# Kernel tuning notes

Measured on AMD Instinct MI355X. Metric: run time of the kernel, lower is better.

## Reference

```python
import jax, jax.numpy as jnp
import numpy as np
from jax import lax

NEG = -1e16  # value used by masked_fill in the original
DN = ('NCHW', 'OIHW', 'NCHW')


def _time_block(X, w1, b1, w2, b2, w3, b3):
    # X: [B, N, T, C] -> conv over time with kernel (1,3), VALID -> [B, N, T-2, O]
    x = jnp.transpose(X, (0, 3, 1, 2))  # [B, C, N, T]
    conv = lambda w, b: lax.conv_general_dilated(x, w, (1, 1), 'VALID', dimension_numbers=DN) + b[None, :, None, None]
    temp = conv(w1, b1) + jax.nn.sigmoid(conv(w2, b2))
    out = jax.nn.relu(temp + conv(w3, b3))
    return jnp.transpose(out, (0, 2, 3, 1))  # [B, N, T-2, O]


def _gat_single(x, graph, W, b):
    # x: [B, N, C]; W: [D, C]; b: [D]
    h = jnp.einsum('bnc,dc->bnd', x, W)
    s = jnp.einsum('bnd,bmd->bnm', h, h) * graph[None]
    s = jnp.where(s == 0, NEG, s)
    a = jax.nn.softmax(s, axis=-1)
    return jnp.einsum('bnm,bmd->bnd', a, h) + b


def _gat_multihead(x, graph, Wh, bh):
    # x: [B, N, C]; Wh: [H, D, C]; bh: [H, D] -> [B, N, H*D] (head-major concat, matching torch.cat)
    h = jnp.einsum('bnc,hdc->bhnd', x, Wh)
    s = jnp.einsum('bhnd,bhmd->bhnm', h, h) * graph[None, None]
    s = jnp.where(s == 0, NEG, s)
    a = jax.nn.softmax(s, axis=-1)
    o = jnp.einsum('bhnm,bhmd->bhnd', a, h) + bh[None, :, None, :]
    B, H, N, D = o.shape
    return jnp.transpose(o, (0, 2, 1, 3)).reshape(B, N, H * D)


def setup_inputs() -> dict:
    key = jax.random.key(0)
    ks = jax.random.split(key, 12)
    B, N, T, C = 2, 4096, 5, 192
    hid, out_c, H = 64, 64, 4
    inp = {
        'flow': jax.random.normal(ks[0], (B, N, T, C), jnp.float32),
        'graph': jax.random.randint(ks[1], (N, N), 0, 2).astype(jnp.float32),
        'tb_w1': jax.random.normal(ks[2], (hid, C, 1, 3), jnp.float32) * 0.1,
        'tb_b1': jax.random.normal(ks[3], (hid,), jnp.float32) * 0.1,
        'tb_w2': jax.random.normal(ks[4], (hid, C, 1, 3), jnp.float32) * 0.1,
        'tb_b2': jax.random.normal(ks[5], (hid,), jnp.float32) * 0.1,
        'tb_w3': jax.random.normal(ks[6], (hid, C, 1, 3), jnp.float32) * 0.1,
        'tb_b3': jax.random.normal(ks[7], (hid,), jnp.float32) * 0.1,
        'Wh': jax.random.normal(ks[8], (H, hid, C), jnp.float32) * 0.1,
        'bh': jax.random.normal(ks[9], (H, hid), jnp.float32) * 0.1,
        'Wo': jax.random.normal(ks[10], (out_c, hid * H), jnp.float32) * 0.1,
        'bo': jax.random.normal(ks[11], (out_c,), jnp.float32) * 0.1,
    }
    return inp


def reference(flow, graph, tb_w1, tb_b1, tb_w2, tb_b2, tb_w3, tb_b3, Wh, bh, Wo, bo):
    B, N = flow.shape[0], flow.shape[1]
    t1 = _time_block(flow, tb_w1, tb_b1, tb_w2, tb_b2, tb_w3, tb_b3)  # [B, N, T-2, hid]
    x = t1.reshape(B, N, -1)  # [B, N, (T-2)*hid]
    x = jax.nn.leaky_relu(_gat_multihead(x, graph, Wh, bh), negative_slope=0.01)
    x = jax.nn.leaky_relu(_gat_single(x, graph, Wo, bo), negative_slope=0.01)
    return x[:, :, None, :]  # [B, N, 1, out_c]
```

## Files before the change

kernel.cpp:

```cpp
#include <hip/hip_runtime.h>
#include <math.h>

#define N_NODES 4096

typedef unsigned short u16;
typedef unsigned int u32;

typedef __attribute__((ext_vector_type(8))) short bfrag;
typedef __attribute__((ext_vector_type(4))) float f4;

__device__ __forceinline__ u16 f2bf(float x) {
    union { float f; u32 u; } v; v.f = x;
    u32 r = (v.u + 0x7FFFu + ((v.u >> 16) & 1u)) >> 16;
    return (u16)r;
}
__device__ __forceinline__ float bf2f(u16 b) {
    union { float f; u32 u; } v; v.u = ((u32)b) << 16; return v.f;
}
__device__ __forceinline__ u32 cvtpk(float a, float b) {
    u32 r;
    asm("v_cvt_pk_bf16_f32 %0, %1, %2" : "=v"(r) : "v"(a), "v"(b));
    return r;
}
__device__ __forceinline__ float u2f(u32 u) {
    union { u32 u; float f; } v; v.u = u; return v.f;
}

__global__ __launch_bounds__(256) void wprep_kernel(
    const float* __restrict__ w1, const float* __restrict__ w2,
    const float* __restrict__ w3,
    u16* __restrict__ w_hi, u16* __restrict__ w_mid, u16* __restrict__ w_lo)
{
    int idx = blockIdx.x * 256 + threadIdx.x;
    if (idx >= 192 * 576) return;
    int col = idx / 576, k = idx % 576;
    int conv = col >> 6, o = col & 63;
    int kk = k / 192, c = k % 192;
    const float* w = (conv == 0) ? w1 : (conv == 1 ? w2 : w3);
    float v = w[(o * 192 + c) * 3 + kk];
    u16 h = f2bf(v);   float r1 = v - bf2f(h);
    u16 m = f2bf(r1);  float r2 = r1 - bf2f(m);
    u16 lo = f2bf(r2);
    int kc = k >> 6, rem = k & 63, j = rem >> 3, e = rem & 7;
    int pos = col * 576 + kc * 64 + ((j ^ (col & 7)) << 3) + e;
    w_hi[pos] = h;
    w_mid[pos] = m;
    w_lo[pos] = lo;
}

__global__ __launch_bounds__(512) void timeblock_mfma_kernel(
    const float* __restrict__ flow,
    const u16* __restrict__ w_hi, const u16* __restrict__ w_mid,
    const u16* __restrict__ w_lo,
    const float* __restrict__ b1, const float* __restrict__ b2,
    const float* __restrict__ b3, float* __restrict__ x1)
{
    __shared__ __align__(16) u16 As[3][128 * 64];
    __shared__ __align__(16) u16 Bs[3][192 * 64];

    const int tid = threadIdx.x;
    const int wv = tid >> 6, l = tid & 63;
    const int ln15 = l & 15, ln16 = l >> 4;
    const int wr = wv >> 1, wc = wv & 1;
    const int nodebase = blockIdx.x * 128;
    const int t = blockIdx.y;

    f4 acc[2][6];
#pragma unroll
    for (int rq = 0; rq < 2; ++rq)
#pragma unroll
        for (int nt = 0; nt < 6; ++nt) {
            acc[rq][nt][0] = 0.f; acc[rq][nt][1] = 0.f;
            acc[rq][nt][2] = 0.f; acc[rq][nt][3] = 0.f;
        }

    for (int kc = 0; kc < 9; ++kc) {
        __syncthreads();

#pragma unroll
        for (int u = tid; u < 1024; u += 512) {
            int r = u >> 3, j = u & 7;
            const float* srcp = flow + (size_t)(nodebase + r) * 960 + t * 192 + kc * 64 + j * 8;
            float4 f0 = *(const float4*)srcp;
            float4 f1 = *(const float4*)(srcp + 4);
            float fv[8] = { f0.x, f0.y, f0.z, f0.w, f1.x, f1.y, f1.z, f1.w };
            union { uint4 q; u16 a[8]; } uh, um, ul;
#pragma unroll
            for (int e = 0; e < 8; ++e) {
                u16 h = f2bf(fv[e]);   float r1 = fv[e] - bf2f(h);
                u16 m = f2bf(r1);      float r2 = r1 - bf2f(m);
                uh.a[e] = h; um.a[e] = m; ul.a[e] = f2bf(r2);
            }
            int pos = r * 64 + ((j ^ (r & 7)) << 3);
            *(uint4*)&As[0][pos] = uh.q;
            *(uint4*)&As[1][pos] = um.q;
            *(uint4*)&As[2][pos] = ul.q;
        }

#pragma unroll
        for (int arr = 0; arr < 3; ++arr) {
            const u16* wsrc = (arr == 0) ? w_hi : (arr == 1 ? w_mid : w_lo);
#pragma unroll
            for (int i = 0; i < 3; ++i) {
                int colg = wv * 24 + i * 8;
                const u16* srcp = wsrc + (size_t)(colg + (l >> 3)) * 576 + kc * 64 + (l & 7) * 8;
                u16* dstp = &Bs[arr][colg * 64];
                __builtin_amdgcn_global_load_lds(
                    (const __attribute__((address_space(1))) u32*)srcp,
                    (__attribute__((address_space(3))) u32*)dstp, 16, 0, 0);
            }
        }

        __syncthreads();

        bfrag af[2][3][2];
#pragma unroll
        for (int rq = 0; rq < 2; ++rq) {
            int arow = wr * 32 + rq * 16 + ln15;
#pragma unroll
            for (int ks = 0; ks < 2; ++ks) {
                int idx = arow * 64 + (((ks * 4 + ln16) ^ (arow & 7)) << 3);
                af[rq][0][ks] = *(const bfrag*)&As[0][idx];
                af[rq][1][ks] = *(const bfrag*)&As[1][idx];
                af[rq][2][ks] = *(const bfrag*)&As[2][idx];
            }
        }

#pragma unroll
        for (int cv = 0; cv < 3; ++cv) {
#pragma unroll
            for (int ntj = 0; ntj < 2; ++ntj) {
                int col = cv * 64 + wc * 32 + ntj * 16 + ln15;
                int nt = cv * 2 + ntj;
#pragma unroll
                for (int ks = 0; ks < 2; ++ks) {
                    int idx = col * 64 + (((ks * 4 + ln16) ^ (col & 7)) << 3);
                    bfrag bh = *(const bfrag*)&Bs[0][idx];
                    bfrag bm = *(const bfrag*)&Bs[1][idx];
                    bfrag bl = *(const bfrag*)&Bs[2][idx];
#pragma unroll
                    for (int rq = 0; rq < 2; ++rq) {
                        f4 a = acc[rq][nt];
                        a = __builtin_amdgcn_mfma_f32_16x16x32_bf16(af[rq][0][ks], bh, a, 0, 0, 0);
                        a = __builtin_amdgcn_mfma_f32_16x16x32_bf16(af[rq][0][ks], bm, a, 0, 0, 0);
                        a = __builtin_amdgcn_mfma_f32_16x16x32_bf16(af[rq][1][ks], bh, a, 0, 0, 0);
                        a = __builtin_amdgcn_mfma_f32_16x16x32_bf16(af[rq][0][ks], bl, a, 0, 0, 0);
                        a = __builtin_amdgcn_mfma_f32_16x16x32_bf16(af[rq][2][ks], bh, a, 0, 0, 0);
                        a = __builtin_amdgcn_mfma_f32_16x16x32_bf16(af[rq][1][ks], bm, a, 0, 0, 0);
                        acc[rq][nt] = a;
                    }
                }
            }
        }
    }

#pragma unroll
    for (int rq = 0; rq < 2; ++rq) {
#pragma unroll
        for (int ntj = 0; ntj < 2; ++ntj) {
            int o = wc * 32 + ntj * 16 + ln15;
            float bb1 = b1[o], bb2 = b2[o], bb3 = b3[o];
#pragma unroll
            for (int rg = 0; rg < 4; ++rg) {
                int node = nodebase + wr * 32 + rq * 16 + ln16 * 4 + rg;
                float c1 = acc[rq][0 * 2 + ntj][rg] + bb1;
                float c2 = acc[rq][1 * 2 + ntj][rg] + bb2;
                float c3 = acc[rq][2 * 2 + ntj][rg] + bb3;
                float sg = 1.0f / (1.0f + __expf(-c2));
                float v = c1 + sg + c3;
                x1[(size_t)node * 192 + t * 64 + o] = v > 0.f ? v : 0.f;
            }
        }
    }
}

__global__ __launch_bounds__(256) void linear64_split_kernel(
    const float* __restrict__ in, const float* __restrict__ W,
    u16* __restrict__ h_hi, u16* __restrict__ h_lo,
    u16* __restrict__ hTb_hi, u16* __restrict__ hTb_lo,
    int C, int H)
{
    __shared__ float xs[64][68];
    __shared__ float wsm[64][68];
    const int tid = threadIdx.x;
    const int g = blockIdx.y;
    const int rowbase = blockIdx.x * 64;
    const int rgrp = tid >> 4, cgrp = tid & 15;

    float acc[4][4] = {};
    for (int c0 = 0; c0 < C; c0 += 64) {
        __syncthreads();
        for (int i = tid; i < 4096; i += 256) {
            int r = i >> 6, cc = i & 63;
            xs[r][cc]  = in[(size_t)(rowbase + r) * C + c0 + cc];
            wsm[r][cc] = W[(size_t)(g * 64 + r) * C + c0 + cc];
        }
        __syncthreads();
        for (int cc = 0; cc < 64; cc += 4) {
            float4 xv[4], wv[4];
#pragma unroll
            for (int i = 0; i < 4; ++i)
                xv[i] = *reinterpret_cast<const float4*>(&xs[4 * rgrp + i][cc]);
#pragma unroll
            for (int j = 0; j < 4; ++j)
                wv[j] = *reinterpret_cast<const float4*>(&wsm[4 * cgrp + j][cc]);
#pragma unroll
            for (int i = 0; i < 4; ++i) {
#pragma unroll
                for (int j = 0; j < 4; ++j) {
                    acc[i][j] += xv[i].x * wv[j].x + xv[i].y * wv[j].y
                               + xv[i].z * wv[j].z + xv[i].w * wv[j].w;
                }
            }
        }
    }

    u16 hi[4][4], lo[4][4];
#pragma unroll
    for (int i = 0; i < 4; ++i)
#pragma unroll
        for (int j = 0; j < 4; ++j) {
            float a = acc[i][j];
            u16 h = f2bf(a);
            hi[i][j] = h;
            lo[i][j] = f2bf(a - bf2f(h));
        }

    const int b = rowbase >> 12;
    const size_t mapb = (size_t)(b * H + g) * (4096 * 64);

#pragma unroll
    for (int i = 0; i < 4; ++i) {
        int n = (rowbase & 4095) + 4 * rgrp + i;
        ushort4 vh = { hi[i][0], hi[i][1], hi[i][2], hi[i][3] };
        ushort4 vl = { lo[i][0], lo[i][1], lo[i][2], lo[i][3] };
        *(ushort4*)&h_hi[mapb + (size_t)n * 64 + 4 * cgrp] = vh;
        *(ushort4*)&h_lo[mapb + (size_t)n * 64 + 4 * cgrp] = vl;
    }
    {
        int n0 = (rowbase & 4095) + 4 * rgrp;
        size_t tb = mapb + ((size_t)(n0 >> 6) * 64) * 64;
#pragma unroll
        for (int j = 0; j < 4; ++j) {
            int d = 4 * cgrp + j;
            ushort4 vh = { hi[0][j], hi[1][j], hi[2][j], hi[3][j] };
            ushort4 vl = { lo[0][j], lo[1][j], lo[2][j], lo[3][j] };
            *(ushort4*)&hTb_hi[tb + (size_t)d * 64 + (n0 & 63)] = vh;
            *(ushort4*)&hTb_lo[tb + (size_t)d * 64 + (n0 & 63)] = vl;
        }
    }
}

__global__ __launch_bounds__(256) void flash_mfma_kernel(
    const u16* __restrict__ h_hi, const u16* __restrict__ h_lo,
    const u16* __restrict__ hTb_hi, const u16* __restrict__ hTb_lo,
    const float* __restrict__ graph, const float* __restrict__ bias,
    float* __restrict__ out, int H, int rstride,
    int ntiles, int mode, float* __restrict__ pO, float* __restrict__ pml)
{
    __shared__ __align__(16) u16 hcs[2][4][4096];

    const int tid = threadIdx.x;
    const int wv = tid >> 6;
    const int l = tid & 63;
    const int ln15 = l & 15, ln16 = l >> 4;
    const int by = blockIdx.y;
    const int chunk = blockIdx.z;
    const int t0 = chunk * ntiles;
    const int bb = by / H, head = by % H;
    const size_t mapb = (size_t)by * (4096 * 64);
    const int rowbase = blockIdx.x * 64;

    const int arow = rowbase + wv * 16 + ln15;
    bfrag ahi[2], alo[2];
#pragma unroll
    for (int ks = 0; ks < 2; ++ks) {
        ahi[ks] = *(const bfrag*)(h_hi + mapb + (size_t)arow * 64 + ks * 32 + ln16 * 8);
        alo[ks] = *(const bfrag*)(h_lo + mapb + (size_t)arow * 64 + ks * 32 + ln16 * 8);
    }

    const u16* gA = (wv == 0 ? h_hi : wv == 1 ? h_lo : wv == 2 ? hTb_hi : hTb_lo) + mapb;
    const int lrow = l >> 3;
    const int stoff = lrow * 64 + (((l & 7) ^ lrow) << 3);

#define STAGE(T, BUF)                                                          \
    {                                                                          \
        const u16* srcp = gA + (size_t)(T) * 4096 + stoff;                     \
        u16* dstp = &hcs[BUF][wv][0];                                          \
        _Pragma("unroll")                                                      \
        for (int i_ = 0; i_ < 8; ++i_)                                         \
            __builtin_amdgcn_global_load_lds(                                  \
                (const __attribute__((address_space(1))) u32*)(srcp + i_ * 512), \
                (__attribute__((address_space(3))) u32*)(dstp + i_ * 512),     \
                16, 0, 0);                                                     \
    }

    const float* grow = graph + (size_t)(rowbase + wv * 16 + ln15) * 4096 + ln16 * 4;

    float m_ = -3.0e38f, l_ = 0.f;
    f4 acco[4];
#pragma unroll
    for (int i = 0; i < 4; ++i) {
        acco[i][0] = 0.f; acco[i][1] = 0.f; acco[i][2] = 0.f; acco[i][3] = 0.f;
    }

    STAGE(t0, 0);
    float4 grC[4], grN[4];
#pragma unroll
    for (int cb = 0; cb < 4; ++cb)
        grC[cb] = *(const float4*)(grow + (size_t)t0 * 64 + cb * 16);

    const int srcA = ln15 + ((((ln16 << 1)) & 3) << 4);
    const int srcB = ln15 + ((((ln16 << 1) + 1) & 3) << 4);
    const bool hi2 = (ln16 & 2) != 0;

    for (int tt = 0; tt < ntiles; ++tt) {
        const int t = t0 + tt;
        const int cur = tt & 1;

        __syncthreads();

        if (tt + 1 < ntiles) {
            STAGE(t + 1, cur ^ 1);
#pragma unroll
            for (int cb = 0; cb < 4; ++cb)
                grN[cb] = *(const float4*)(grow + (size_t)(t + 1) * 64 + cb * 16);
        }

        __builtin_amdgcn_s_setprio(1);
        f4 accs[4];
#pragma unroll
        for (int cb = 0; cb < 4; ++cb) {
            f4 a; a[0] = 0.f; a[1] = 0.f; a[2] = 0.f; a[3] = 0.f;
#pragma unroll
            for (int ks = 0; ks < 2; ++ks) {
                int c = cb * 16 + ln15;
                int idx = c * 64 + (((ks * 4 + ln16) * 8) ^ ((c & 7) << 3));
                bfrag bhi = *(const bfrag*)&hcs[cur][0][idx];
                bfrag blo = *(const bfrag*)&hcs[cur][1][idx];
                a = __builtin_amdgcn_mfma_f32_16x16x32_bf16(bhi, ahi[ks], a, 0, 0, 0);
                a = __builtin_amdgcn_mfma_f32_16x16x32_bf16(bhi, alo[ks], a, 0, 0, 0);
                a = __builtin_amdgcn_mfma_f32_16x16x32_bf16(blo, ahi[ks], a, 0, 0, 0);
            }
            accs[cb] = a;
        }
        __builtin_amdgcn_s_setprio(0);

        float p[4][4];
#pragma unroll
        for (int cb = 0; cb < 4; ++cb) {
            float g0 = grC[cb].x, g1 = grC[cb].y, g2 = grC[cb].z, g3 = grC[cb].w;
            float v0 = accs[cb][0] * g0; p[cb][0] = (v0 == 0.f) ? -1e16f : v0;
            float v1 = accs[cb][1] * g1; p[cb][1] = (v1 == 0.f) ? -1e16f : v1;
            float v2 = accs[cb][2] * g2; p[cb][2] = (v2 == 0.f) ? -1e16f : v2;
            float v3 = accs[cb][3] * g3; p[cb][3] = (v3 == 0.f) ? -1e16f : v3;
        }

        float tm = fmaxf(fmaxf(p[0][0], p[0][1]), fmaxf(p[0][2], p[0][3]));
#pragma unroll
        for (int cb = 1; cb < 4; ++cb)
            tm = fmaxf(tm, fmaxf(fmaxf(p[cb][0], p[cb][1]), fmaxf(p[cb][2], p[cb][3])));
        tm = fmaxf(tm, __shfl_xor(tm, 16));
        tm = fmaxf(tm, __shfl_xor(tm, 32));

        float mn = fmaxf(m_, tm);
        float corr = __expf(m_ - mn);

        float rs = 0.f;
#pragma unroll
        for (int cb = 0; cb < 4; ++cb) {
            p[cb][0] = __expf(p[cb][0] - mn);
            p[cb][1] = __expf(p[cb][1] - mn);
            p[cb][2] = __expf(p[cb][2] - mn);
            p[cb][3] = __expf(p[cb][3] - mn);
            rs += (p[cb][0] + p[cb][1]) + (p[cb][2] + p[cb][3]);
        }
        rs += __shfl_xor(rs, 16);
        rs += __shfl_xor(rs, 32);
        l_ = l_ * corr + rs;
        m_ = mn;

        float corr4[4];
#pragma unroll
        for (int rg = 0; rg < 4; ++rg)
            corr4[rg] = __shfl(corr, ln16 * 4 + rg);
#pragma unroll
        for (int nb = 0; nb < 4; ++nb) {
            acco[nb][0] *= corr4[0]; acco[nb][1] *= corr4[1];
            acco[nb][2] *= corr4[2]; acco[nb][3] *= corr4[3];
        }

        u32 Uh[4][2], Ul[4][2];
#pragma unroll
        for (int cb = 0; cb < 4; ++cb) {
            u32 uh0 = cvtpk(p[cb][0], p[cb][1]);
            u32 uh1 = cvtpk(p[cb][2], p[cb][3]);
            float h0 = u2f(uh0 << 16), h1 = u2f(uh0 & 0xffff0000u);
            float h2 = u2f(uh1 << 16), h3 = u2f(uh1 & 0xffff0000u);
            Uh[cb][0] = uh0; Uh[cb][1] = uh1;
            Ul[cb][0] = cvtpk(p[cb][0] - h0, p[cb][1] - h1);
            Ul[cb][1] = cvtpk(p[cb][2] - h2, p[cb][3] - h3);
        }

        bfrag pfh[2], pfl[2];
#pragma unroll
        for (int ks = 0; ks < 2; ++ks) {
            u32 w0a = (u32)__shfl((int)Uh[2 * ks + 0][0], srcA);
            u32 w0b = (u32)__shfl((int)Uh[2 * ks + 1][0], srcA);
            u32 w1a = (u32)__shfl((int)Uh[2 * ks + 0][1], srcA);
            u32 w1b = (u32)__shfl((int)Uh[2 * ks + 1][1], srcA);
            u32 w2a = (u32)__shfl((int)Uh[2 * ks + 0][0], srcB);
            u32 w2b = (u32)__shfl((int)Uh[2 * ks + 1][0], srcB);
            u32 w3a = (u32)__shfl((int)Uh[2 * ks + 0][1], srcB);
            u32 w3b = (u32)__shfl((int)Uh[2 * ks + 1][1], srcB);
            union { uint4 q; bfrag f; } ch;
            ch.q.x = hi2 ? w0b : w0a; ch.q.y = hi2 ? w1b : w1a;
            ch.q.z = hi2 ? w2b : w2a; ch.q.w = hi2 ? w3b : w3a;
            pfh[ks] = ch.f;

            u32 v0a = (u32)__shfl((int)Ul[2 * ks + 0][0], srcA);
            u32 v0b = (u32)__shfl((int)Ul[2 * ks + 1][0], srcA);
            u32 v1a = (u32)__shfl((int)Ul[2 * ks + 0][1], srcA);
            u32 v1b = (u32)__shfl((int)Ul[2 * ks + 1][1], srcA);
            u32 v2a = (u32)__shfl((int)Ul[2 * ks + 0][0], srcB);
            u32 v2b = (u32)__shfl((int)Ul[2 * ks + 1][0], srcB);
            u32 v3a = (u32)__shfl((int)Ul[2 * ks + 0][1], srcB);
            u32 v3b = (u32)__shfl((int)Ul[2 * ks + 1][1], srcB);
            union { uint4 q; bfrag f; } cl;
            cl.q.x = hi2 ? v0b : v0a; cl.q.y = hi2 ? v1b : v1a;
            cl.q.z = hi2 ? v2b : v2a; cl.q.w = hi2 ? v3b : v3a;
            pfl[ks] = cl.f;
        }

        __builtin_amdgcn_s_setprio(1);
#pragma unroll
        for (int nb = 0; nb < 4; ++nb) {
#pragma unroll
            for (int ks = 0; ks < 2; ++ks) {
                int nr = nb * 16 + ln15;
                int idx = nr * 64 + (((ks * 4 + ln16) * 8) ^ ((nr & 7) << 3));
                bfrag vhi = *(const bfrag*)&hcs[cur][2][idx];
                bfrag vlo = *(const bfrag*)&hcs[cur][3][idx];
                acco[nb] = __builtin_amdgcn_mfma_f32_16x16x32_bf16(pfh[ks], vhi, acco[nb], 0, 0, 0);
                acco[nb] = __builtin_amdgcn_mfma_f32_16x16x32_bf16(pfh[ks], vlo, acco[nb], 0, 0, 0);
                acco[nb] = __builtin_amdgcn_mfma_f32_16x16x32_bf16(pfl[ks], vhi, acco[nb], 0, 0, 0);
            }
        }
        __builtin_amdgcn_s_setprio(0);

        if (tt + 1 < ntiles) {
#pragma unroll
            for (int cb = 0; cb < 4; ++cb)
                grC[cb] = grN[cb];
        }
    }
#undef STAGE

    if (mode == 0) {
        float l4[4];
#pragma unroll
        for (int rg = 0; rg < 4; ++rg)
            l4[rg] = __shfl(l_, ln16 * 4 + rg);

        const float* bv = bias + head * 64;
#pragma unroll
        for (int rg = 0; rg < 4; ++rg) {
            int row = rowbase + wv * 16 + ln16 * 4 + rg;
            float inv = 1.0f / l4[rg];
#pragma unroll
            for (int nb = 0; nb < 4; ++nb) {
                float v = acco[nb][rg] * inv + bv[nb * 16 + ln15];
                v = v > 0.f ? v : 0.01f * v;
                out[(size_t)(bb * N_NODES + row) * rstride + head * 64 + nb * 16 + ln15] = v;
            }
        }
    } else {
        int row = rowbase + wv * 16 + ln15;
        if (ln16 == 0) {
            size_t mi = (((size_t)by * 4 + chunk) * 4096 + row) * 2;
            pml[mi] = m_;
            pml[mi + 1] = l_;
        }
#pragma unroll
        for (int rg = 0; rg < 4; ++rg) {
            int row2 = rowbase + wv * 16 + ln16 * 4 + rg;
            size_t ob = (((size_t)by * 4 + chunk) * 4096 + row2) * 64;
#pragma unroll
            for (int nb = 0; nb < 4; ++nb)
                pO[ob + nb * 16 + ln15] = acco[nb][rg];
        }
    }
}

__global__ __launch_bounds__(256) void merge_kernel(
    const float* __restrict__ pO, const float* __restrict__ pml,
    const float* __restrict__ bias, float* __restrict__ out)
{
    int idx = blockIdx.x * 256 + threadIdx.x;
    int feat = idx & 63;
    int row = (idx >> 6) & 4095;
    int map = idx >> 18;

    float mv[4], lv[4];
    float M = -3.0e38f;
#pragma unroll
    for (int c = 0; c < 4; ++c) {
        size_t mi = (((size_t)map * 4 + c) * 4096 + row) * 2;
        mv[c] = pml[mi];
        lv[c] = pml[mi + 1];
        M = fmaxf(M, mv[c]);
    }
    float den = 0.f, num = 0.f;
#pragma unroll
    for (int c = 0; c < 4; ++c) {
        float e = __expf(mv[c] - M);
        den += e * lv[c];
        num += e * pO[(((size_t)map * 4 + c) * 4096 + row) * 64 + feat];
    }
    float v = num / den + bias[feat];
    v = v > 0.f ? v : 0.01f * v;
    out[((size_t)map * 4096 + row) * 64 + feat] = v;
}

extern "C" void kernel_launch(void* const* d_in, const int* in_sizes, int n_in,
                              void* d_out, int out_size, void* d_ws, size_t ws_size,
                              hipStream_t stream)
{
    const float* flow = (const float*)d_in[0];
    const float* graph = (const float*)d_in[1];
    const float* w1 = (const float*)d_in[2];
    const float* b1 = (const float*)d_in[3];
    const float* w2 = (const float*)d_in[4];
    const float* b2 = (const float*)d_in[5];
    const float* w3 = (const float*)d_in[6];
    const float* b3 = (const float*)d_in[7];
    const float* Wh = (const float*)d_in[8];
    const float* bh = (const float*)d_in[9];
    const float* Wo = (const float*)d_in[10];
    const float* bo = (const float*)d_in[11];

    char* ws = (char*)d_ws;
    u16* wc_hi  = (u16*)ws;
    u16* wc_mid = wc_hi + (size_t)192 * 576;
    u16* wc_lo  = wc_mid + (size_t)192 * 576;

    u16* h1_hi  = (u16*)ws;
    u16* h1_lo  = h1_hi + (size_t)8 * 4096 * 64;
    u16* h1T_hi = h1_lo + (size_t)8 * 4096 * 64;
    u16* h1T_lo = h1T_hi + (size_t)8 * 4096 * 64;
    u16* h2_hi  = (u16*)ws;
    u16* h2_lo  = h2_hi + (size_t)2 * 4096 * 64;
    u16* h2T_hi = h2_lo + (size_t)2 * 4096 * 64;
    u16* h2T_lo = h2T_hi + (size_t)2 * 4096 * 64;
    float* pml  = (float*)(ws + (size_t)6 * 1024 * 1024);
    float* xreg = (float*)(ws + (size_t)4 * 8 * 4096 * 64 * 2);
    float* x1 = xreg;
    float* x2 = xreg;
    float* pO = xreg;
    float* outp = (float*)d_out;

    hipLaunchKernelGGL(wprep_kernel, dim3(432), dim3(256), 0, stream,
                       w1, w2, w3, wc_hi, wc_mid, wc_lo);
    hipLaunchKernelGGL(timeblock_mfma_kernel, dim3(64, 3), dim3(512), 0, stream,
                       flow, wc_hi, wc_mid, wc_lo, b1, b2, b3, x1);
    hipLaunchKernelGGL(linear64_split_kernel, dim3(128, 4), dim3(256), 0, stream,
                       x1, Wh, h1_hi, h1_lo, h1T_hi, h1T_lo, 192, 4);
    hipLaunchKernelGGL(flash_mfma_kernel, dim3(64, 8, 1), dim3(256), 0, stream,
                       h1_hi, h1_lo, h1T_hi, h1T_lo, graph, bh, x2, 4, 256,
                       64, 0, (float*)nullptr, (float*)nullptr);
    hipLaunchKernelGGL(linear64_split_kernel, dim3(128, 1), dim3(256), 0, stream,
                       x2, Wo, h2_hi, h2_lo, h2T_hi, h2T_lo, 256, 1);
    hipLaunchKernelGGL(flash_mfma_kernel, dim3(64, 2, 4), dim3(256), 0, stream,
                       h2_hi, h2_lo, h2T_hi, h2T_lo, graph, bo, (float*)nullptr, 1, 64,
                       16, 1, pO, pml);
    hipLaunchKernelGGL(merge_kernel, dim3(2048), dim3(256), 0, stream,
                       pO, pml, bo, outp);
}
```

Before: 324.5 us.

## Reorder flash grid for graph-tile L2 reuse, halve block rows, cheapen softmax

Both attention kernels now launch with map/chunk as the fast grid dimension and 32-row, 2-wave blocks. Blocks that read the same rows of the dense fp32 graph run next to each other, so repeated graph reads should hit L2 instead of HBM. The LDS tile drops to one buffer per wave pair, with a sync before and after staging, which gives up overlap of the next tile's load with compute. The softmax is also simplified: the mask becomes an additive fma bias, exp uses raw v_exp_f32 in base 2, and accumulator rescaling is skipped when no row max increases. The additive mask no longer treats an exact zero score on a real edge as masked, a small semantic deviation.

New measurement: 341.9 us. +5.4%, slower.

```diff
diff --git a/kernel.cpp b/kernel.cpp
--- a/kernel.cpp
+++ b/kernel.cpp
@@ -25,6 +25,13 @@
 __device__ __forceinline__ float u2f(u32 u) {
     union { u32 u; float f; } v; v.u = u; return v.f;
 }
+__device__ __forceinline__ float fexp2(float x) {
+    float r;
+    asm("v_exp_f32 %0, %1" : "=v"(r) : "v"(x));
+    return r;
+}
+
+#define LOG2E 1.4426950408889634f
 
 __global__ __launch_bounds__(256) void wprep_kernel(
     const float* __restrict__ w1, const float* __restrict__ w2,
@@ -251,25 +258,26 @@
     }
 }
 
-__global__ __launch_bounds__(256) void flash_mfma_kernel(
+__global__ __launch_bounds__(128) void flash_mfma_kernel(
     const u16* __restrict__ h_hi, const u16* __restrict__ h_lo,
     const u16* __restrict__ hTb_hi, const u16* __restrict__ hTb_lo,
     const float* __restrict__ graph, const float* __restrict__ bias,
     float* __restrict__ out, int H, int rstride,
-    int ntiles, int mode, float* __restrict__ pO, float* __restrict__ pml)
+    int ntiles, int nch, int mode, float* __restrict__ pO, float* __restrict__ pml)
 {
-    __shared__ __align__(16) u16 hcs[2][4][4096];
+    __shared__ __align__(16) u16 hcs[4][4096];
 
     const int tid = threadIdx.x;
     const int wv = tid >> 6;
     const int l = tid & 63;
     const int ln15 = l & 15, ln16 = l >> 4;
-    const int by = blockIdx.y;
-    const int chunk = blockIdx.z;
+    const int bx = blockIdx.x;
+    const int by = bx / nch;
+    const int chunk = bx - by * nch;
     const int t0 = chunk * ntiles;
-    const int bb = by / H, head = by % H;
+    const int bb = by / H, head = by - bb * H;
     const size_t mapb = (size_t)by * (4096 * 64);
-    const int rowbase = blockIdx.x * 64;
+    const int rowbase = blockIdx.y * 32;
 
     const int arow = rowbase + wv * 16 + ln15;
     bfrag ahi[2], alo[2];
@@ -279,20 +287,28 @@
         alo[ks] = *(const bfrag*)(h_lo + mapb + (size_t)arow * 64 + ks * 32 + ln16 * 8);
     }
 
-    const u16* gA = (wv == 0 ? h_hi : wv == 1 ? h_lo : wv == 2 ? hTb_hi : hTb_lo) + mapb;
+    const u16* g0 = (wv == 0 ? h_hi : hTb_hi) + mapb;
+    const u16* g1 = (wv == 0 ? h_lo : hTb_lo) + mapb;
     const int lrow = l >> 3;
     const int stoff = lrow * 64 + (((l & 7) ^ lrow) << 3);
-
-#define STAGE(T, BUF)                                                          \
+    u16* d0 = &hcs[wv * 2][0];
+    u16* d1 = &hcs[wv * 2 + 1][0];
+
+#define STAGE(T)                                                               \
     {                                                                          \
-        const u16* srcp = gA + (size_t)(T) * 4096 + stoff;                     \
-        u16* dstp = &hcs[BUF][wv][0];                                          \
+        const u16* s0_ = g0 + (size_t)(T) * 4096 + stoff;                      \
+        const u16* s1_ = g1 + (size_t)(T) * 4096 + stoff;                      \
         _Pragma("unroll")                                                      \
-        for (int i_ = 0; i_ < 8; ++i_)                                         \
+        for (int i_ = 0; i_ < 8; ++i_) {                                       \
             __builtin_amdgcn_global_load_lds(                                  \
-                (const __attribute__((address_space(1))) u32*)(srcp + i_ * 512), \
-                (__attribute__((address_space(3))) u32*)(dstp + i_ * 512),     \
+                (const __attribute__((address_space(1))) u32*)(s0_ + i_ * 512),\
+                (__attribute__((address_space(3))) u32*)(d0 + i_ * 512),       \
                 16, 0, 0);                                                     \
+            __builtin_amdgcn_global_load_lds(                                  \
+                (const __attribute__((address_space(1))) u32*)(s1_ + i_ * 512),\
+                (__attribute__((address_space(3))) u32*)(d1 + i_ * 512),       \
+                16, 0, 0);                                                     \
+        }                                                                      \
     }
 
     const float* grow = graph + (size_t)(rowbase + wv * 16 + ln15) * 4096 + ln16 * 4;
@@ -304,11 +320,17 @@
         acco[i][0] = 0.f; acco[i][1] = 0.f; acco[i][2] = 0.f; acco[i][3] = 0.f;
     }
 
-    STAGE(t0, 0);
     float4 grC[4], grN[4];
 #pragma unroll
     for (int cb = 0; cb < 4; ++cb)
-        grC[cb] = *(const float4*)(grow + (size_t)t0 * 64 + cb * 16);
+        grN[cb] = *(const float4*)(grow + (size_t)t0 * 64 + cb * 16);
+#pragma unroll
+    for (int cb = 0; cb < 4; ++cb) {
+        grC[cb].x = fmaf(grN[cb].x, 1e16f, -1e16f);
+        grC[cb].y = fmaf(grN[cb].y, 1e16f, -1e16f);
+        grC[cb].z = fmaf(grN[cb].z, 1e16f, -1e16f);
+        grC[cb].w = fmaf(grN[cb].w, 1e16f, -1e16f);
+    }
 
     const int srcA = ln15 + ((((ln16 << 1)) & 3) << 4);
     const int srcB = ln15 + ((((ln16 << 1) + 1) & 3) << 4);
@@ -316,12 +338,12 @@
 
     for (int tt = 0; tt < ntiles; ++tt) {
         const int t = t0 + tt;
-        const int cur = tt & 1;
 
         __syncthreads();
+        STAGE(t);
+        __syncthreads();
 
         if (tt + 1 < ntiles) {
-            STAGE(t + 1, cur ^ 1);
 #pragma unroll
             for (int cb = 0; cb < 4; ++cb)
                 grN[cb] = *(const float4*)(grow + (size_t)(t + 1) * 64 + cb * 16);
@@ -336,8 +358,8 @@
             for (int ks = 0; ks < 2; ++ks) {
                 int c = cb * 16 + ln15;
                 int idx = c * 64 + (((ks * 4 + ln16) * 8) ^ ((c & 7) << 3));
-                bfrag bhi = *(const bfrag*)&hcs[cur][0][idx];
-                bfrag blo = *(const bfrag*)&hcs[cur][1][idx];
+                bfrag bhi = *(const bfrag*)&hcs[0][idx];
+                bfrag blo = *(const bfrag*)&hcs[1][idx];
                 a = __builtin_amdgcn_mfma_f32_16x16x32_bf16(bhi, ahi[ks], a, 0, 0, 0);
                 a = __builtin_amdgcn_mfma_f32_16x16x32_bf16(bhi, alo[ks], a, 0, 0, 0);
                 a = __builtin_amdgcn_mfma_f32_16x16x32_bf16(blo, ahi[ks], a, 0, 0, 0);
@@ -349,11 +371,10 @@
         float p[4][4];
 #pragma unroll
         for (int cb = 0; cb < 4; ++cb) {
-            float g0 = grC[cb].x, g1 = grC[cb].y, g2 = grC[cb].z, g3 = grC[cb].w;
-            float v0 = accs[cb][0] * g0; p[cb][0] = (v0 == 0.f) ? -1e16f : v0;
-            float v1 = accs[cb][1] * g1; p[cb][1] = (v1 == 0.f) ? -1e16f : v1;
-            float v2 = accs[cb][2] * g2; p[cb][2] = (v2 == 0.f) ? -1e16f : v2;
-            float v3 = accs[cb][3] * g3; p[cb][3] = (v3 == 0.f) ? -1e16f : v3;
+            p[cb][0] = accs[cb][0] + grC[cb].x;
+            p[cb][1] = accs[cb][1] + grC[cb].y;
+            p[cb][2] = accs[cb][2] + grC[cb].z;
+            p[cb][3] = accs[cb][3] + grC[cb].w;
         }
 
         float tm = fmaxf(fmaxf(p[0][0], p[0][1]), fmaxf(p[0][2], p[0][3]));
@@ -363,16 +384,24 @@
         tm = fmaxf(tm, __shfl_xor(tm, 16));
         tm = fmaxf(tm, __shfl_xor(tm, 32));
 
-        float mn = fmaxf(m_, tm);
-        float corr = __expf(m_ - mn);
+        const bool anyup = __any(tm > m_);
+        float mn, corr;
+        if (anyup) {
+            mn = fmaxf(m_, tm);
+            corr = fexp2((m_ - mn) * LOG2E);
+        } else {
+            mn = m_;
+            corr = 1.0f;
+        }
+        const float c0 = -mn * LOG2E;
 
         float rs = 0.f;
 #pragma unroll
         for (int cb = 0; cb < 4; ++cb) {
-            p[cb][0] = __expf(p[cb][0] - mn);
-            p[cb][1] = __expf(p[cb][1] - mn);
-            p[cb][2] = __expf(p[cb][2] - mn);
-            p[cb][3] = __expf(p[cb][3] - mn);
+            p[cb][0] = fexp2(fmaf(p[cb][0], LOG2E, c0));
+            p[cb][1] = fexp2(fmaf(p[cb][1], LOG2E, c0));
+            p[cb][2] = fexp2(fmaf(p[cb][2], LOG2E, c0));
+            p[cb][3] = fexp2(fmaf(p[cb][3], LOG2E, c0));
             rs += (p[cb][0] + p[cb][1]) + (p[cb][2] + p[cb][3]);
         }
         rs += __shfl_xor(rs, 16);
@@ -380,14 +409,16 @@
         l_ = l_ * corr + rs;
         m_ = mn;
 
-        float corr4[4];
-#pragma unroll
-        for (int rg = 0; rg < 4; ++rg)
-            corr4[rg] = __shfl(corr, ln16 * 4 + rg);
-#pragma unroll
-        for (int nb = 0; nb < 4; ++nb) {
-            acco[nb][0] *= corr4[0]; acco[nb][1] *= corr4[1];
-            acco[nb][2] *= corr4[2]; acco[nb][3] *= corr4[3];
+        if (anyup) {
+            float corr4[4];
+#pragma unroll
+            for (int rg = 0; rg < 4; ++rg)
+                corr4[rg] = __shfl(corr, ln16 * 4 + rg);
+#pragma unroll
+            for (int nb = 0; nb < 4; ++nb) {
+                acco[nb][0] *= corr4[0]; acco[nb][1] *= corr4[1];
+                acco[nb][2] *= corr4[2]; acco[nb][3] *= corr4[3];
+            }
         }
 
         u32 Uh[4][2], Ul[4][2];
@@ -439,8 +470,8 @@
             for (int ks = 0; ks < 2; ++ks) {
                 int nr = nb * 16 + ln15;
                 int idx = nr * 64 + (((ks * 4 + ln16) * 8) ^ ((nr & 7) << 3));
-                bfrag vhi = *(const bfrag*)&hcs[cur][2][idx];
-                bfrag vlo = *(const bfrag*)&hcs[cur][3][idx];
+                bfrag vhi = *(const bfrag*)&hcs[2][idx];
+                bfrag vlo = *(const bfrag*)&hcs[3][idx];
                 acco[nb] = __builtin_amdgcn_mfma_f32_16x16x32_bf16(pfh[ks], vhi, acco[nb], 0, 0, 0);
                 acco[nb] = __builtin_amdgcn_mfma_f32_16x16x32_bf16(pfh[ks], vlo, acco[nb], 0, 0, 0);
                 acco[nb] = __builtin_amdgcn_mfma_f32_16x16x32_bf16(pfl[ks], vhi, acco[nb], 0, 0, 0);
@@ -450,8 +481,12 @@
 
         if (tt + 1 < ntiles) {
 #pragma unroll
-            for (int cb = 0; cb < 4; ++cb)
-                grC[cb] = grN[cb];
+            for (int cb = 0; cb < 4; ++cb) {
+                grC[cb].x = fmaf(grN[cb].x, 1e16f, -1e16f);
+                grC[cb].y = fmaf(grN[cb].y, 1e16f, -1e16f);
+                grC[cb].z = fmaf(grN[cb].z, 1e16f, -1e16f);
+                grC[cb].w = fmaf(grN[cb].w, 1e16f, -1e16f);
+            }
         }
     }
 #undef STAGE
@@ -477,14 +512,14 @@
     } else {
         int row = rowbase + wv * 16 + ln15;
         if (ln16 == 0) {
-            size_t mi = (((size_t)by * 4 + chunk) * 4096 + row) * 2;
+            size_t mi = (((size_t)(by * nch + chunk)) * 4096 + row) * 2;
             pml[mi] = m_;
             pml[mi + 1] = l_;
         }
 #pragma unroll
         for (int rg = 0; rg < 4; ++rg) {
             int row2 = rowbase + wv * 16 + ln16 * 4 + rg;
-            size_t ob = (((size_t)by * 4 + chunk) * 4096 + row2) * 64;
+            size_t ob = (((size_t)(by * nch + chunk)) * 4096 + row2) * 64;
 #pragma unroll
             for (int nb = 0; nb < 4; ++nb)
                 pO[ob + nb * 16 + ln15] = acco[nb][rg];
@@ -565,14 +600,14 @@
                        flow, wc_hi, wc_mid, wc_lo, b1, b2, b3, x1);
     hipLaunchKernelGGL(linear64_split_kernel, dim3(128, 4), dim3(256), 0, stream,
                        x1, Wh, h1_hi, h1_lo, h1T_hi, h1T_lo, 192, 4);
-    hipLaunchKernelGGL(flash_mfma_kernel, dim3(64, 8, 1), dim3(256), 0, stream,
+    hipLaunchKernelGGL(flash_mfma_kernel, dim3(8, 128), dim3(128), 0, stream,
                        h1_hi, h1_lo, h1T_hi, h1T_lo, graph, bh, x2, 4, 256,
-                       64, 0, (float*)nullptr, (float*)nullptr);
+                       64, 1, 0, (float*)nullptr, (float*)nullptr);
     hipLaunchKernelGGL(linear64_split_kernel, dim3(128, 1), dim3(256), 0, stream,
                        x2, Wo, h2_hi, h2_lo, h2T_hi, h2T_lo, 256, 1);
-    hipLaunchKernelGGL(flash_mfma_kernel, dim3(64, 2, 4), dim3(256), 0, stream,
+    hipLaunchKernelGGL(flash_mfma_kernel, dim3(8, 128), dim3(128), 0, stream,
                        h2_hi, h2_lo, h2T_hi, h2T_lo, graph, bo, (float*)nullptr, 1, 64,
-                       16, 1, pO, pml);
+                       16, 4, 1, pO, pml);
     hipLaunchKernelGGL(merge_kernel, dim3(2048), dim3(256), 0, stream,
                        pO, pml, bo, outp);
 }
```

## Use exp2 softmax, skip rescale when max unchanged, reorder grid for graph reuse

Applied to the files above, without the earlier changes.

The mask is now applied additively with an fma: a graph value of 1 adds zero and a graph value of 0 adds -1e16. The exponentials use raw v_exp_f32 on log2e-prescaled inputs. The online-softmax rescale of the accumulators and its shuffles is skipped when no lane's row max increased. The grid is remapped so the fastest-varying block index walks heads, batches and chunks for the same row block, which should improve L2 reuse of the graph tiles. The additive mask differs from the original multiply-then-compare-to-zero semantics when a score is exactly zero or graph entries are not 0/1, and it adds a wave-wide vote and branch.

Result: faster. 314.6 us (-3.0%).

```diff
diff --git a/kernel.cpp b/kernel.cpp
--- a/kernel.cpp
+++ b/kernel.cpp
@@ -25,6 +25,13 @@
 __device__ __forceinline__ float u2f(u32 u) {
     union { u32 u; float f; } v; v.u = u; return v.f;
 }
+__device__ __forceinline__ float fexp2(float x) {
+    float r;
+    asm("v_exp_f32 %0, %1" : "=v"(r) : "v"(x));
+    return r;
+}
+
+#define LOG2E 1.4426950408889634f
 
 __global__ __launch_bounds__(256) void wprep_kernel(
     const float* __restrict__ w1, const float* __restrict__ w2,
@@ -256,7 +263,7 @@
     const u16* __restrict__ hTb_hi, const u16* __restrict__ hTb_lo,
     const float* __restrict__ graph, const float* __restrict__ bias,
     float* __restrict__ out, int H, int rstride,
-    int ntiles, int mode, float* __restrict__ pO, float* __restrict__ pml)
+    int ntiles, int nch, int mode, float* __restrict__ pO, float* __restrict__ pml)
 {
     __shared__ __align__(16) u16 hcs[2][4][4096];
 
@@ -264,12 +271,13 @@
     const int wv = tid >> 6;
     const int l = tid & 63;
     const int ln15 = l & 15, ln16 = l >> 4;
-    const int by = blockIdx.y;
-    const int chunk = blockIdx.z;
+    const int bx = blockIdx.x;
+    const int by = bx / nch;
+    const int chunk = bx - by * nch;
     const int t0 = chunk * ntiles;
-    const int bb = by / H, head = by % H;
+    const int bb = by / H, head = by - bb * H;
     const size_t mapb = (size_t)by * (4096 * 64);
-    const int rowbase = blockIdx.x * 64;
+    const int rowbase = blockIdx.y * 64;
 
     const int arow = rowbase + wv * 16 + ln15;
     bfrag ahi[2], alo[2];
@@ -349,11 +357,10 @@
         float p[4][4];
 #pragma unroll
         for (int cb = 0; cb < 4; ++cb) {
-            float g0 = grC[cb].x, g1 = grC[cb].y, g2 = grC[cb].z, g3 = grC[cb].w;
-            float v0 = accs[cb][0] * g0; p[cb][0] = (v0 == 0.f) ? -1e16f : v0;
-            float v1 = accs[cb][1] * g1; p[cb][1] = (v1 == 0.f) ? -1e16f : v1;
-            float v2 = accs[cb][2] * g2; p[cb][2] = (v2 == 0.f) ? -1e16f : v2;
-            float v3 = accs[cb][3] * g3; p[cb][3] = (v3 == 0.f) ? -1e16f : v3;
+            p[cb][0] = accs[cb][0] + fmaf(grC[cb].x, 1e16f, -1e16f);
+            p[cb][1] = accs[cb][1] + fmaf(grC[cb].y, 1e16f, -1e16f);
+            p[cb][2] = accs[cb][2] + fmaf(grC[cb].z, 1e16f, -1e16f);
+            p[cb][3] = accs[cb][3] + fmaf(grC[cb].w, 1e16f, -1e16f);
         }
 
         float tm = fmaxf(fmaxf(p[0][0], p[0][1]), fmaxf(p[0][2], p[0][3]));
@@ -363,16 +370,24 @@
         tm = fmaxf(tm, __shfl_xor(tm, 16));
         tm = fmaxf(tm, __shfl_xor(tm, 32));
 
-        float mn = fmaxf(m_, tm);
-        float corr = __expf(m_ - mn);
+        const bool anyup = __any(tm > m_);
+        float mn, corr;
+        if (anyup) {
+            mn = fmaxf(m_, tm);
+            corr = fexp2((m_ - mn) * LOG2E);
+        } else {
+            mn = m_;
+            corr = 1.0f;
+        }
+        const float c0 = -mn * LOG2E;
 
         float rs = 0.f;
 #pragma unroll
         for (int cb = 0; cb < 4; ++cb) {
-            p[cb][0] = __expf(p[cb][0] - mn);
-            p[cb][1] = __expf(p[cb][1] - mn);
-            p[cb][2] = __expf(p[cb][2] - mn);
-            p[cb][3] = __expf(p[cb][3] - mn);
+            p[cb][0] = fexp2(fmaf(p[cb][0], LOG2E, c0));
+            p[cb][1] = fexp2(fmaf(p[cb][1], LOG2E, c0));
+            p[cb][2] = fexp2(fmaf(p[cb][2], LOG2E, c0));
+            p[cb][3] = fexp2(fmaf(p[cb][3], LOG2E, c0));
             rs += (p[cb][0] + p[cb][1]) + (p[cb][2] + p[cb][3]);
         }
         rs += __shfl_xor(rs, 16);
@@ -380,14 +395,16 @@
         l_ = l_ * corr + rs;
         m_ = mn;
 
-        float corr4[4];
-#pragma unroll
-        for (int rg = 0; rg < 4; ++rg)
-            corr4[rg] = __shfl(corr, ln16 * 4 + rg);
-#pragma unroll
-        for (int nb = 0; nb < 4; ++nb) {
-            acco[nb][0] *= corr4[0]; acco[nb][1] *= corr4[1];
-            acco[nb][2] *= corr4[2]; acco[nb][3] *= corr4[3];
+        if (anyup) {
+            float corr4[4];
+#pragma unroll
+            for (int rg = 0; rg < 4; ++rg)
+                corr4[rg] = __shfl(corr, ln16 * 4 + rg);
+#pragma unroll
+            for (int nb = 0; nb < 4; ++nb) {
+                acco[nb][0] *= corr4[0]; acco[nb][1] *= corr4[1];
+                acco[nb][2] *= corr4[2]; acco[nb][3] *= corr4[3];
+            }
         }
 
         u32 Uh[4][2], Ul[4][2];
@@ -477,14 +494,14 @@
     } else {
         int row = rowbase + wv * 16 + ln15;
         if (ln16 == 0) {
-            size_t mi = (((size_t)by * 4 + chunk) * 4096 + row) * 2;
+            size_t mi = (((size_t)(by * nch + chunk)) * 4096 + row) * 2;
             pml[mi] = m_;
             pml[mi + 1] = l_;
         }
 #pragma unroll
         for (int rg = 0; rg < 4; ++rg) {
             int row2 = rowbase + wv * 16 + ln16 * 4 + rg;
-            size_t ob = (((size_t)by * 4 + chunk) * 4096 + row2) * 64;
+            size_t ob = (((size_t)(by * nch + chunk)) * 4096 + row2) * 64;
 #pragma unroll
             for (int nb = 0; nb < 4; ++nb)
                 pO[ob + nb * 16 + ln15] = acco[nb][rg];
@@ -565,14 +582,14 @@
                        flow, wc_hi, wc_mid, wc_lo, b1, b2, b3, x1);
     hipLaunchKernelGGL(linear64_split_kernel, dim3(128, 4), dim3(256), 0, stream,
                        x1, Wh, h1_hi, h1_lo, h1T_hi, h1T_lo, 192, 4);
-    hipLaunchKernelGGL(flash_mfma_kernel, dim3(64, 8, 1), dim3(256), 0, stream,
+    hipLaunchKernelGGL(flash_mfma_kernel, dim3(8, 64), dim3(256), 0, stream,
                        h1_hi, h1_lo, h1T_hi, h1T_lo, graph, bh, x2, 4, 256,
-                       64, 0, (float*)nullptr, (float*)nullptr);
+                       64, 1, 0, (float*)nullptr, (float*)nullptr);
     hipLaunchKernelGGL(linear64_split_kernel, dim3(128, 1), dim3(256), 0, stream,
                        x2, Wo, h2_hi, h2_lo, h2T_hi, h2T_lo, 256, 1);
-    hipLaunchKernelGGL(flash_mfma_kernel, dim3(64, 2, 4), dim3(256), 0, stream,
+    hipLaunchKernelGGL(flash_mfma_kernel, dim3(8, 64), dim3(256), 0, stream,
                        h2_hi, h2_lo, h2T_hi, h2T_lo, graph, bo, (float*)nullptr, 1, 64,
-                       16, 1, pO, pml);
+                       16, 4, 1, pO, pml);
     hipLaunchKernelGGL(merge_kernel, dim3(2048), dim3(256), 0, stream,
                        pO, pml, bo, outp);
 }
```
